# Optimization experiments

Measured on AMD Instinct MI355X. Metric: run time of the kernel, lower is better.

The kernel has to match this reference:

```python
import jax, jax.numpy as jnp
import numpy as np

N_SRC = 100000
N_DST = 100000
D = 128
K = 10
E_SAMP = 1000000


def setup_inputs() -> dict:
    key = jax.random.key(0)
    k1, k2, k3, k4, k5, k6, k7 = jax.random.split(key, 7)
    h_src = jax.random.normal(k1, (N_SRC, D), dtype=jnp.float32)
    weight = jax.random.normal(k2, (D, D), dtype=jnp.float32) * (1.0 / np.sqrt(D))
    bias = jax.random.normal(k3, (D,), dtype=jnp.float32) * 0.01
    sampled_src = jax.random.randint(k4, (E_SAMP,), 0, N_SRC, dtype=jnp.int64)
    sampled_dst = jnp.sort(jax.random.randint(k5, (E_SAMP,), 0, N_DST, dtype=jnp.int64))
    out_deg = jax.random.randint(k6, (N_SRC,), 0, 64, dtype=jnp.int32)
    in_deg = jax.random.randint(k7, (N_DST,), 0, 64, dtype=jnp.int32)
    return {
        "h_src": h_src,
        "weight": weight,
        "bias": bias,
        "sampled_src": sampled_src,
        "sampled_dst": sampled_dst,
        "out_deg": out_deg,
        "in_deg": in_deg,
    }


def reference(h_src, weight, bias, sampled_src, sampled_dst, out_deg, in_deg):
    # pre-aggregation normalization: out_degree^-0.5 (clamped to >=1)
    norm_src = jnp.clip(out_deg.astype(h_src.dtype), 1.0, None) ** -0.5  # [N_SRC]
    feat_src = h_src * norm_src[:, None]                                  # [N_SRC, D]
    # fused gather + (pre-sampled) neighbor sum: copy_src -> segment_sum
    msg = feat_src[sampled_src]                                           # [E_SAMP, D]
    agg = jax.ops.segment_sum(msg, sampled_dst, num_segments=N_DST,
                              indices_are_sorted=True)                    # [N_DST, D]
    rst = agg @ weight                                                    # [N_DST, D]
    # post normalization: clamp(in_degree, 1, k)^-0.5
    norm_dst = jnp.clip(in_deg.astype(rst.dtype), 1.0, float(K)) ** -0.5  # [N_DST]
    rst = rst * norm_dst[:, None] + bias
    return rst
```

## Files before the change

kernel.cpp:

```cpp
#include <hip/hip_runtime.h>
#include <hip/hip_bf16.h>
#include <cstdint>

#define NDIM 128
#define KCLAMP 10.0f

using bf16x8 = __attribute__((ext_vector_type(8))) short;
using f32x4  = __attribute__((ext_vector_type(4))) float;
using f32x2  = __attribute__((ext_vector_type(2))) float;

__device__ __forceinline__ uint16_t f2bf(float f) {
    uint32_t u = __float_as_uint(f);
    uint32_t r = (u + 0x7fffu + ((u >> 16) & 1u)) >> 16;
    return (uint16_t)r;
}
__device__ __forceinline__ float bf_lo(uint32_t v) { return __uint_as_float(v << 16); }
__device__ __forceinline__ float bf_hi(uint32_t v) { return __uint_as_float(v & 0xffff0000u); }

__global__ void k_prep(const float* __restrict__ W, uint16_t* __restrict__ wfrag,
                       const int* __restrict__ sdst, int E,
                       int* __restrict__ row_start, int ndst, int wfBlocks) {
    int b = blockIdx.x;
    int tid = threadIdx.x;
    if (b < wfBlocks) {
        int t = b * 256 + tid;
        if (t >= NDIM * NDIM) return;
        int i    = t & 7;
        int lane = (t >> 3) & 63;
        int s    = (t >> 9) & 3;
        int n    = t >> 11;
        int k    = s * 32 + 8 * (lane >> 4) + i;
        int col  = n * 16 + (lane & 15);
        wfrag[t] = f2bf(W[k * NDIM + col]);
    } else {
        int d = (b - wfBlocks) * 256 + tid;
        if (d > ndst) return;
        int lo = 0, hi = E;
        while (lo < hi) {
            int mid = (lo + hi) >> 1;
            if (sdst[mid] < d) lo = mid + 1; else hi = mid;
        }
        row_start[d] = lo;
    }
}

__global__ __launch_bounds__(256) void k1_gemm(
        const float* __restrict__ h, const int* __restrict__ odeg,
        const uint16_t* __restrict__ wfrag, uint16_t* __restrict__ trans, int M) {
    __shared__ uint16_t Ws[NDIM * NDIM];
    int tx = threadIdx.x;
    for (int i = tx; i < NDIM * NDIM / 8; i += 256)
        ((int4*)Ws)[i] = ((const int4*)wfrag)[i];
    __syncthreads();

    int wave = tx >> 6, lane = tx & 63;
    int g = lane >> 4;
    int r0 = blockIdx.x * 64 + wave * 16;
    int arow = r0 + (lane & 15);
    if (arow >= M) arow = M - 1;
    float nrm = rsqrtf(fmaxf((float)odeg[arow], 1.0f));
    const float4* Arow = (const float4*)(h + (size_t)arow * NDIM);

    f32x4 acc[8];
#pragma unroll
    for (int n = 0; n < 8; ++n) acc[n] = (f32x4){0.f, 0.f, 0.f, 0.f};

#pragma unroll
    for (int s = 0; s < 4; ++s) {
        float4 a0 = Arow[s * 8 + g * 2];
        float4 a1 = Arow[s * 8 + g * 2 + 1];
        bf16x8 af;
        af[0] = (short)f2bf(a0.x * nrm);
        af[1] = (short)f2bf(a0.y * nrm);
        af[2] = (short)f2bf(a0.z * nrm);
        af[3] = (short)f2bf(a0.w * nrm);
        af[4] = (short)f2bf(a1.x * nrm);
        af[5] = (short)f2bf(a1.y * nrm);
        af[6] = (short)f2bf(a1.z * nrm);
        af[7] = (short)f2bf(a1.w * nrm);
#pragma unroll
        for (int n = 0; n < 8; ++n) {
            bf16x8 bfr = *(const bf16x8*)(Ws + (((n * 4 + s) * 64 + lane) << 3));
            acc[n] = __builtin_amdgcn_mfma_f32_16x16x32_bf16(af, bfr, acc[n], 0, 0, 0);
        }
    }

    int colL = lane & 15;
    int rowbase = r0 + g * 4;
#pragma unroll
    for (int n = 0; n < 8; ++n) {
#pragma unroll
        for (int r = 0; r < 4; ++r) {
            int row = rowbase + r;
            if (row < M)
                trans[(size_t)row * NDIM + n * 16 + colL] = f2bf(acc[n][r]);
        }
    }
}

__global__ __launch_bounds__(256) void k2_gather(
        const uint16_t* __restrict__ trans,
        const int* __restrict__ ssrc, const int* __restrict__ row_start,
        const float* __restrict__ bias, const int* __restrict__ ideg,
        float* __restrict__ out, int ndst) {
    constexpr int U = 8;
    int gtid = blockIdx.x * blockDim.x + threadIdx.x;
    int wave = gtid >> 6;
    int lane = threadIdx.x & 63;
    int sub  = lane >> 4;
    int li   = lane & 15;
    int nwaves = (gridDim.x * blockDim.x) >> 6;

    float4 b0 = ((const float4*)bias)[li * 2];
    float4 b1 = ((const float4*)bias)[li * 2 + 1];

    for (int d0 = wave * 4; d0 < ndst; d0 += nwaves * 4) {
        int d = d0 + sub;
        int valid = (d < ndst);
        int s = 0, e = 0;
        if (valid) { s = row_start[d]; e = row_start[d + 1]; }
        int elast = (e > s) ? (e - 1) : 0;

        f32x2 acc[4];
#pragma unroll
        for (int k = 0; k < 4; ++k) acc[k] = (f32x2){0.f, 0.f};

        int idxv[U];
#pragma unroll
        for (int u = 0; u < U; ++u) idxv[u] = ssrc[min(s + u, elast)];

        int pos = s;
        while (__any(pos < e)) {
            uint4 v[U];
#pragma unroll
            for (int u = 0; u < U; ++u)
                v[u] = *(const uint4*)(trans + (size_t)idxv[u] * NDIM + li * 8);

            int npos = pos + U;
#pragma unroll
            for (int u = 0; u < U; ++u) idxv[u] = ssrc[min(npos + u, elast)];

#pragma unroll
            for (int u = 0; u < U; ++u) {
                if (pos + u < e) {
                    f32x2 t0 = {bf_lo(v[u].x), bf_hi(v[u].x)};
                    f32x2 t1 = {bf_lo(v[u].y), bf_hi(v[u].y)};
                    f32x2 t2 = {bf_lo(v[u].z), bf_hi(v[u].z)};
                    f32x2 t3 = {bf_lo(v[u].w), bf_hi(v[u].w)};
                    acc[0] += t0; acc[1] += t1; acc[2] += t2; acc[3] += t3;
                }
            }
            pos = npos;
        }

        if (valid) {
            float nrm = rsqrtf(fminf(fmaxf((float)ideg[d], 1.0f), KCLAMP));
            float4 o0, o1;
            o0.x = acc[0][0] * nrm + b0.x;
            o0.y = acc[0][1] * nrm + b0.y;
            o0.z = acc[1][0] * nrm + b0.z;
            o0.w = acc[1][1] * nrm + b0.w;
            o1.x = acc[2][0] * nrm + b1.x;
            o1.y = acc[2][1] * nrm + b1.y;
            o1.z = acc[3][0] * nrm + b1.z;
            o1.w = acc[3][1] * nrm + b1.w;
            ((float4*)out)[(size_t)d * (NDIM / 4) + li * 2]     = o0;
            ((float4*)out)[(size_t)d * (NDIM / 4) + li * 2 + 1] = o1;
        }
    }
}

__global__ void k_rowptr(const int* __restrict__ sdst, int E,
                         int* __restrict__ row_start, int ndst) {
    int d = blockIdx.x * blockDim.x + threadIdx.x;
    if (d > ndst) return;
    int lo = 0, hi = E;
    while (lo < hi) {
        int mid = (lo + hi) >> 1;
        if (sdst[mid] < d) lo = mid + 1; else hi = mid;
    }
    row_start[d] = lo;
}

__global__ void k_agg_f32(const float* __restrict__ h, const int* __restrict__ odeg,
                          const int* __restrict__ ssrc, const int* __restrict__ row_start,
                          float* __restrict__ agg, int ndst) {
    int gtid = blockIdx.x * blockDim.x + threadIdx.x;
    int wave = gtid >> 6;
    int lane = threadIdx.x & 63;
    int nwaves = (gridDim.x * blockDim.x) >> 6;
    for (int d = wave; d < ndst; d += nwaves) {
        int s = row_start[d], e = row_start[d + 1];
        float a0 = 0.f, a1 = 0.f;
        for (int i = s; i < e; i++) {
            int s0 = ssrc[i];
            float nrm = rsqrtf(fmaxf((float)odeg[s0], 1.0f));
            float2 v = ((const float2*)h)[(size_t)s0 * (NDIM / 2) + lane];
            a0 += v.x * nrm;
            a1 += v.y * nrm;
        }
        float2 o; o.x = a0; o.y = a1;
        ((float2*)agg)[(size_t)d * (NDIM / 2) + lane] = o;
    }
}

__global__ __launch_bounds__(256) void k_gemm_f32(float* __restrict__ io,
                                                  const float* __restrict__ W,
                                                  const float* __restrict__ bias,
                                                  const int* __restrict__ ideg, int M) {
    __shared__ float Wsf[NDIM][NDIM];
    int tx = threadIdx.x;
    {
        const float4* Wv = (const float4*)W;
        float4* Wsv = (float4*)&Wsf[0][0];
        for (int i = tx; i < NDIM * NDIM / 4; i += 256) Wsv[i] = Wv[i];
    }
    __syncthreads();
    int cg = tx & 31, rg = tx >> 5;
    int r0 = blockIdx.x * 64 + rg * 8, c0 = cg * 4;
    float acc[8][4];
#pragma unroll
    for (int r = 0; r < 8; ++r)
#pragma unroll
        for (int c = 0; c < 4; ++c) acc[r][c] = 0.f;
    for (int k4 = 0; k4 < NDIM / 4; ++k4) {
        float4 wk0 = *(const float4*)&Wsf[4 * k4 + 0][c0];
        float4 wk1 = *(const float4*)&Wsf[4 * k4 + 1][c0];
        float4 wk2 = *(const float4*)&Wsf[4 * k4 + 2][c0];
        float4 wk3 = *(const float4*)&Wsf[4 * k4 + 3][c0];
#pragma unroll
        for (int r = 0; r < 8; ++r) {
            int row = r0 + r;
            if (row < M) {
                float4 a = ((const float4*)io)[(size_t)row * (NDIM / 4) + k4];
                acc[r][0] += a.x * wk0.x + a.y * wk1.x + a.z * wk2.x + a.w * wk3.x;
                acc[r][1] += a.x * wk0.y + a.y * wk1.y + a.z * wk2.y + a.w * wk3.y;
                acc[r][2] += a.x * wk0.z + a.y * wk1.z + a.z * wk2.z + a.w * wk3.z;
                acc[r][3] += a.x * wk0.w + a.y * wk1.w + a.z * wk2.w + a.w * wk3.w;
            }
        }
    }
    __syncthreads();
    float4 b = *(const float4*)&bias[c0];
#pragma unroll
    for (int r = 0; r < 8; ++r) {
        int row = r0 + r;
        if (row < M) {
            float nrm = rsqrtf(fminf(fmaxf((float)ideg[row], 1.0f), KCLAMP));
            float4 o;
            o.x = acc[r][0] * nrm + b.x;
            o.y = acc[r][1] * nrm + b.y;
            o.z = acc[r][2] * nrm + b.z;
            o.w = acc[r][3] * nrm + b.w;
            ((float4*)io)[(size_t)row * (NDIM / 4) + cg] = o;
        }
    }
}

extern "C" void kernel_launch(void* const* d_in, const int* in_sizes, int n_in,
                              void* d_out, int out_size, void* d_ws, size_t ws_size,
                              hipStream_t stream) {
    const float* h_src  = (const float*)d_in[0];
    const float* weight = (const float*)d_in[1];
    const float* bias   = (const float*)d_in[2];
    const int*   ssrc   = (const int*)d_in[3];
    const int*   sdst   = (const int*)d_in[4];
    const int*   odeg   = (const int*)d_in[5];
    const int*   ideg   = (const int*)d_in[6];
    float* out = (float*)d_out;

    int E    = in_sizes[3];
    int nsrc = in_sizes[0] / NDIM;
    int ndst = out_size / NDIM;

    int*      row_start = (int*)d_ws;
    uint16_t* wfrag = (uint16_t*)((char*)d_ws + ((size_t)1 << 20));
    uint16_t* trans = (uint16_t*)((char*)d_ws + ((size_t)2 << 20));
    size_t need = ((size_t)2 << 20) + (size_t)nsrc * NDIM * 2;

    if (ws_size >= need) {
        int wfBlocks = (NDIM * NDIM + 255) / 256;
        int rpBlocks = (ndst + 1 + 255) / 256;
        k_prep<<<wfBlocks + rpBlocks, 256, 0, stream>>>(
            weight, wfrag, sdst, E, row_start, ndst, wfBlocks);
        k1_gemm<<<(nsrc + 63) / 64, 256, 0, stream>>>(h_src, odeg, wfrag, trans, nsrc);
        k2_gather<<<2048, 256, 0, stream>>>(trans, ssrc, row_start, bias, ideg, out, ndst);
    } else {
        k_rowptr<<<(ndst + 1 + 255) / 256, 256, 0, stream>>>(sdst, E, row_start, ndst);
        k_agg_f32<<<2048, 256, 0, stream>>>(h_src, odeg, ssrc, row_start, out, ndst);
        k_gemm_f32<<<(ndst + 63) / 64, 256, 0, stream>>>(out, weight, bias, ideg, ndst);
    }
}
```

Before: 74.10 us.

## Slice transformed features into 16-column panels and gather per panel

The GEMM output is now stored as eight column-major slices of 16 bf16 columns each, so every slice is nsrc*32 bytes. The gather kernel assigns each block to one slice and a chunk of destination rows. Eight lanes split a row's edges and two lanes split the 16 columns, with a shuffle reduction at the end. The aim is to make the randomly gathered working set per slice (about 3.2MB) small enough to stay cache-resident and to lift L2 hit rates. The cost is that each edge index is reloaded eight times across slices, along with extra shuffle reductions and narrower 32-byte loads per edge. Nontemporal hints are also added for index loads and output stores.

```diff
diff --git a/kernel.cpp b/kernel.cpp
--- a/kernel.cpp
+++ b/kernel.cpp
@@ -46,7 +46,8 @@
 
 __global__ __launch_bounds__(256) void k1_gemm(
         const float* __restrict__ h, const int* __restrict__ odeg,
-        const uint16_t* __restrict__ wfrag, uint16_t* __restrict__ trans, int M) {
+        const uint16_t* __restrict__ wfrag, uint16_t* __restrict__ trans,
+        int M, int nsrc) {
     __shared__ uint16_t Ws[NDIM * NDIM];
     int tx = threadIdx.x;
     for (int i = tx; i < NDIM * NDIM / 8; i += 256)
@@ -89,11 +90,12 @@
     int rowbase = r0 + g * 4;
 #pragma unroll
     for (int n = 0; n < 8; ++n) {
+        uint16_t* tslice = trans + (size_t)n * nsrc * 16;
 #pragma unroll
         for (int r = 0; r < 4; ++r) {
             int row = rowbase + r;
             if (row < M)
-                trans[(size_t)row * NDIM + n * 16 + colL] = f2bf(acc[n][r]);
+                tslice[(size_t)row * 16 + colL] = f2bf(acc[n][r]);
         }
     }
 }
@@ -102,70 +104,84 @@
         const uint16_t* __restrict__ trans,
         const int* __restrict__ ssrc, const int* __restrict__ row_start,
         const float* __restrict__ bias, const int* __restrict__ ideg,
-        float* __restrict__ out, int ndst) {
-    constexpr int U = 8;
-    int gtid = blockIdx.x * blockDim.x + threadIdx.x;
-    int wave = gtid >> 6;
-    int lane = threadIdx.x & 63;
-    int sub  = lane >> 4;
-    int li   = lane & 15;
-    int nwaves = (gridDim.x * blockDim.x) >> 6;
-
-    float4 b0 = ((const float4*)bias)[li * 2];
-    float4 b1 = ((const float4*)bias)[li * 2 + 1];
-
-    for (int d0 = wave * 4; d0 < ndst; d0 += nwaves * 4) {
-        int d = d0 + sub;
-        int valid = (d < ndst);
-        int s = 0, e = 0;
-        if (valid) { s = row_start[d]; e = row_start[d + 1]; }
-        int elast = (e > s) ? (e - 1) : 0;
-
-        f32x2 acc[4];
-#pragma unroll
-        for (int k = 0; k < 4; ++k) acc[k] = (f32x2){0.f, 0.f};
-
-        int idxv[U];
-#pragma unroll
-        for (int u = 0; u < U; ++u) idxv[u] = ssrc[min(s + u, elast)];
-
-        int pos = s;
+        float* __restrict__ out, int ndst, int nsrc, int DPB) {
+    int bid  = blockIdx.x;
+    int s    = bid & 7;
+    int chunk = bid >> 3;
+    int tx   = threadIdx.x;
+    int wave = tx >> 6, lane = tx & 63;
+    int sub  = lane >> 3;
+    int eo   = (lane >> 1) & 3;
+    int hb   = lane & 1;
+
+    const uint16_t* sbase = trans + (size_t)s * nsrc * 16;
+
+    f32x4 bA = *(const f32x4*)(bias + s * 16 + hb * 8);
+    f32x4 bB = *(const f32x4*)(bias + s * 16 + hb * 8 + 4);
+
+    int dstart = chunk * DPB;
+    int dend   = min(dstart + DPB, ndst);
+
+    for (int db = dstart + wave * 8; db < dend; db += 32) {
+        int d = db + sub;
+        int valid = (d < dend);
+        int sg = 0, e = 0;
+        if (valid) {
+            sg = __builtin_nontemporal_load(row_start + d);
+            e  = __builtin_nontemporal_load(row_start + d + 1);
+        }
+        int elast = (e > sg) ? (e - 1) : 0;
+
+        float a[8];
+#pragma unroll
+        for (int k = 0; k < 8; ++k) a[k] = 0.f;
+
+        int pos = sg;
+        int i0 = __builtin_nontemporal_load(ssrc + min(pos + eo, elast));
+        int i1 = __builtin_nontemporal_load(ssrc + min(pos + 4 + eo, elast));
+
         while (__any(pos < e)) {
-            uint4 v[U];
-#pragma unroll
-            for (int u = 0; u < U; ++u)
-                v[u] = *(const uint4*)(trans + (size_t)idxv[u] * NDIM + li * 8);
-
-            int npos = pos + U;
-#pragma unroll
-            for (int u = 0; u < U; ++u) idxv[u] = ssrc[min(npos + u, elast)];
-
-#pragma unroll
-            for (int u = 0; u < U; ++u) {
-                if (pos + u < e) {
-                    f32x2 t0 = {bf_lo(v[u].x), bf_hi(v[u].x)};
-                    f32x2 t1 = {bf_lo(v[u].y), bf_hi(v[u].y)};
-                    f32x2 t2 = {bf_lo(v[u].z), bf_hi(v[u].z)};
-                    f32x2 t3 = {bf_lo(v[u].w), bf_hi(v[u].w)};
-                    acc[0] += t0; acc[1] += t1; acc[2] += t2; acc[3] += t3;
-                }
+            uint4 v0 = *(const uint4*)(sbase + (size_t)i0 * 16 + hb * 8);
+            uint4 v1 = *(const uint4*)(sbase + (size_t)i1 * 16 + hb * 8);
+            int np = pos + 8;
+            i0 = __builtin_nontemporal_load(ssrc + min(np + eo, elast));
+            i1 = __builtin_nontemporal_load(ssrc + min(np + 4 + eo, elast));
+            if (pos + eo < e) {
+                a[0] += bf_lo(v0.x); a[1] += bf_hi(v0.x);
+                a[2] += bf_lo(v0.y); a[3] += bf_hi(v0.y);
+                a[4] += bf_lo(v0.z); a[5] += bf_hi(v0.z);
+                a[6] += bf_lo(v0.w); a[7] += bf_hi(v0.w);
             }
-            pos = npos;
-        }
-
-        if (valid) {
-            float nrm = rsqrtf(fminf(fmaxf((float)ideg[d], 1.0f), KCLAMP));
-            float4 o0, o1;
-            o0.x = acc[0][0] * nrm + b0.x;
-            o0.y = acc[0][1] * nrm + b0.y;
-            o0.z = acc[1][0] * nrm + b0.z;
-            o0.w = acc[1][1] * nrm + b0.w;
-            o1.x = acc[2][0] * nrm + b1.x;
-            o1.y = acc[2][1] * nrm + b1.y;
-            o1.z = acc[3][0] * nrm + b1.z;
-            o1.w = acc[3][1] * nrm + b1.w;
-            ((float4*)out)[(size_t)d * (NDIM / 4) + li * 2]     = o0;
-            ((float4*)out)[(size_t)d * (NDIM / 4) + li * 2 + 1] = o1;
+            if (pos + 4 + eo < e) {
+                a[0] += bf_lo(v1.x); a[1] += bf_hi(v1.x);
+                a[2] += bf_lo(v1.y); a[3] += bf_hi(v1.y);
+                a[4] += bf_lo(v1.z); a[5] += bf_hi(v1.z);
+                a[6] += bf_lo(v1.w); a[7] += bf_hi(v1.w);
+            }
+            pos = np;
+        }
+
+#pragma unroll
+        for (int k = 0; k < 8; ++k) {
+            a[k] += __shfl_xor(a[k], 2, 64);
+            a[k] += __shfl_xor(a[k], 4, 64);
+        }
+
+        if (eo == 0 && valid) {
+            float nrm = rsqrtf(fminf(fmaxf((float)__builtin_nontemporal_load(ideg + d),
+                                           1.0f), KCLAMP));
+            f32x4 o0, o1;
+            o0[0] = a[0] * nrm + bA[0];
+            o0[1] = a[1] * nrm + bA[1];
+            o0[2] = a[2] * nrm + bA[2];
+            o0[3] = a[3] * nrm + bA[3];
+            o1[0] = a[4] * nrm + bB[0];
+            o1[1] = a[5] * nrm + bB[1];
+            o1[2] = a[6] * nrm + bB[2];
+            o1[3] = a[7] * nrm + bB[3];
+            float* dst = out + (size_t)d * NDIM + s * 16 + hb * 8;
+            __builtin_nontemporal_store(o0, (f32x4*)dst);
+            __builtin_nontemporal_store(o1, (f32x4*)(dst + 4));
         }
     }
 }
@@ -283,8 +299,12 @@
         int rpBlocks = (ndst + 1 + 255) / 256;
         k_prep<<<wfBlocks + rpBlocks, 256, 0, stream>>>(
             weight, wfrag, sdst, E, row_start, ndst, wfBlocks);
-        k1_gemm<<<(nsrc + 63) / 64, 256, 0, stream>>>(h_src, odeg, wfrag, trans, nsrc);
-        k2_gather<<<2048, 256, 0, stream>>>(trans, ssrc, row_start, bias, ideg, out, ndst);
+        k1_gemm<<<(nsrc + 63) / 64, 256, 0, stream>>>(h_src, odeg, wfrag, trans,
+                                                      nsrc, nsrc);
+        int CPB = 256;
+        int DPB = (ndst + CPB - 1) / CPB;
+        k2_gather<<<8 * CPB, 256, 0, stream>>>(trans, ssrc, row_start, bias, ideg,
+                                               out, ndst, nsrc, DPB);
     } else {
         k_rowptr<<<(ndst + 1 + 255) / 256, 256, 0, stream>>>(sdst, E, row_start, ndst);
         k_agg_f32<<<2048, 256, 0, stream>>>(h_src, odeg, ssrc, row_start, out, ndst);
```

After: 155.4 us. +109.7%, slower.
